# Optimization experiments

Measured on AMD Instinct MI355X. Metric: run time of the kernel, lower is better.

Reference implementation:

```python
import jax, jax.numpy as jnp
import numpy as np
from jax import lax

H = 512      # hidden_size (== embed dim)
K = 128      # attr_size
V = 32000    # output_size (vocab)
ANUM = 20    # aspect_num = len(aspect_ids)//100
N, B = 64, 32
T, S, A = 256, 32, 5


def setup_inputs() -> dict:
    key = jax.random.key(0)
    ks = jax.random.split(key, 32)
    f = lambda i, shape, s=0.02: (jax.random.normal(ks[i], shape, jnp.float32) * s)
    inp = {
        "input_seq": jax.random.randint(ks[0], (N, B), 0, V, jnp.int32),
        "last_hidden": jax.random.normal(ks[1], (1, B, H), jnp.float32),
        "encoder_out1": jax.random.normal(ks[2], (T, B, H), jnp.float32),
        "encoder_out2": jax.random.normal(ks[3], (S, B, H), jnp.float32),
        "encoder_out3": jax.random.normal(ks[4], (A, B, K), jnp.float32),
        "encoder_out4": jax.random.normal(ks[5], (A, B, ANUM), jnp.float32),
        "aspect_ids": jax.random.randint(ks[6], (100 * ANUM,), 0, V, jnp.int32),
        # learned parameters
        "emb": f(7, (V, H)),
        "gru_Wih": f(8, (3 * H, H)), "gru_Whh": f(9, (3 * H, H)),
        "gru_bih": f(10, (3 * H,)), "gru_bhh": f(11, (3 * H,)),
        "attn_W": f(12, (H, 2 * H)), "attn_b": f(13, (H,)), "attn_v": f(14, (H,)),
        "attr_W": f(15, (H, H + K)), "attr_b": f(16, (H,)), "attr_v": f(17, (H,)),
        "concat_W": f(18, (H, 3 * H + K)), "concat_b": f(19, (H,)),
        "out_W": f(20, (V, H)), "out_b": f(21, (V,)),
        "gate_W": f(22, (ANUM, 2 * H + ANUM)), "gate_b": f(23, (ANUM,)),
        "proj_W": f(24, (ANUM, 2 * ANUM)), "proj_b": f(25, (ANUM,)),
    }
    return inp


def _gru(x, h0, Wih, Whh, bih, bhh):
    # x: (N,B,H); h0: (B,H). PyTorch gate order: reset, update, new.
    def step(h, xt):
        gi = xt @ Wih.T + bih
        gh = h @ Whh.T + bhh
        ir, iz, inn = jnp.split(gi, 3, axis=-1)
        hr, hz, hn = jnp.split(gh, 3, axis=-1)
        r = jax.nn.sigmoid(ir + hr)
        z = jax.nn.sigmoid(iz + hz)
        n = jnp.tanh(inn + r * hn)
        h_new = (1.0 - z) * n + z * h
        return h_new, h_new
    hT, ys = lax.scan(step, h0, x)
    return ys, hT


def _attn(hidden, enc, W, b, v):
    # Faithful to Attn/AttributeAttn: energies[b,n,t] = tanh(v . (W @ cat(hidden[n,b], enc[t,b]) + b))
    # W @ cat = hidden @ Wh^T + enc @ We^T; dot with v distributes -> avoid (T,N,B,*) blowup.
    Hh = hidden.shape[-1]
    Wh, We = W[:, :Hh], W[:, Hh:]
    a = hidden @ (Wh.T @ v) + jnp.dot(b, v)   # (N,B)
    c = enc @ (We.T @ v)                       # (T,B)
    e = jnp.tanh(a.T[:, :, None] + c.T[:, None, :])  # (B,N,T)
    return jax.nn.softmax(e, axis=2)


def reference(input_seq, last_hidden, encoder_out1, encoder_out2, encoder_out3,
              encoder_out4, aspect_ids, emb, gru_Wih, gru_Whh, gru_bih, gru_bhh,
              attn_W, attn_b, attn_v, attr_W, attr_b, attr_v, concat_W, concat_b,
              out_W, out_b, gate_W, gate_b, proj_W, proj_b):
    seq_len = input_seq.shape[0]
    embedded = emb[input_seq]                                   # (N,B,H), dropout=eval noop
    rnn_output, hT = _gru(embedded, last_hidden[0], gru_Wih, gru_Whh, gru_bih, gru_bhh)
    hidden = hT[None]                                           # (1,B,H)

    aw1 = _attn(rnn_output, encoder_out1, attn_W, attn_b, attn_v)   # (B,N,T)
    ctx1 = jnp.einsum('bnt,tbh->nbh', aw1, encoder_out1)
    aw2 = _attn(rnn_output, encoder_out2, attn_W, attn_b, attn_v)   # (B,N,S)
    ctx2 = jnp.einsum('bns,sbh->nbh', aw2, encoder_out2)
    aw3 = _attn(rnn_output, encoder_out3, attr_W, attr_b, attr_v)   # (B,N,A)
    ctx3 = jnp.einsum('bna,abk->nbk', aw3, encoder_out3)

    concat_input = jnp.concatenate([rnn_output, ctx1, ctx2, ctx3], axis=2)
    concat_output = jnp.tanh(concat_input @ concat_W.T + concat_b)  # (N,B,H)
    output = concat_output @ out_W.T + out_b                        # (N,B,V)

    e4 = jnp.concatenate([encoder_out4[0], encoder_out4[1]], axis=-1)  # (B,2*ANUM)
    e4 = e4 @ proj_W.T + proj_b                                        # (B,ANUM)
    e4 = jnp.broadcast_to(e4[None], (seq_len,) + e4.shape)             # (N,B,ANUM)

    gate = jnp.tanh(jnp.concatenate([embedded, rnn_output, e4], axis=2) @ gate_W.T + gate_b)
    vals = jnp.tile(gate, (1, 1, 100))                                 # (N,B,100*ANUM)
    output = output.at[:, :, aspect_ids].add(vals)
    return output, hidden, aw1, aw2, aw3, gate
```

## Files before the change

kernel.cpp:

```cpp
#include <hip/hip_runtime.h>
#include <hip/hip_bf16.h>

#define HDIM 512
#define KA   128
#define VOC  32000
#define ANUMC 20
#define NSEQ 64
#define BATCH 32
#define TLEN 256
#define SLEN 32
#define ALEN 5
#define NB   2048
#define CIN  1664
#define G3H  1536
#define GB   64

typedef __bf16 bf16;
typedef bf16 v8bf __attribute__((ext_vector_type(8)));
typedef float v4f __attribute__((ext_vector_type(4)));

#define DEV __device__ __forceinline__

DEV float sigmoidf_(float x) { return 1.f / (1.f + expf(-x)); }

__global__ void k_zero(int* bar) {
  for (int i = threadIdx.x; i < GB * 32; i += 256) bar[i] = 0;
}

__global__ void k_init0(float* addtab, int* colnz) {
  int i = blockIdx.x * 256 + threadIdx.x;
  if (i < VOC * ANUMC) addtab[i] = 0.f;
  if (i < VOC) colnz[i] = 0;
}
__global__ void k_init1(const int* __restrict__ ids, float* addtab, int* colnz) {
  for (int k = threadIdx.x; k < 2000; k += 256) {
    int j = ids[k];
    atomicAdd(addtab + (size_t)j * ANUMC + (k % ANUMC), 1.0f);
    colnz[j] = 1;
  }
}

__global__ void k_vec(const float* __restrict__ attn_W, const float* __restrict__ attn_b,
                      const float* __restrict__ attn_v,
                      const float* __restrict__ attr_W, const float* __restrict__ attr_b,
                      const float* __restrict__ attr_v,
                      const float* __restrict__ enc4, const float* __restrict__ pW,
                      const float* __restrict__ pb, float* __restrict__ misc) {
  int tid = threadIdx.x;
  int blk = blockIdx.x;
  if (blk == 0) {
    for (int i = tid; i < 512; i += 256) {
      float s = 0.f;
      for (int j = 0; j < 512; ++j) s += attn_W[j * 1024 + i] * attn_v[j];
      misc[i] = s;
    }
  } else if (blk == 1) {
    for (int i = tid; i < 512; i += 256) {
      float s = 0.f;
      for (int j = 0; j < 512; ++j) s += attn_W[j * 1024 + 512 + i] * attn_v[j];
      misc[512 + i] = s;
    }
  } else if (blk == 2) {
    for (int i = tid; i < 512; i += 256) {
      float s = 0.f;
      for (int j = 0; j < 512; ++j) s += attr_W[j * 640 + i] * attr_v[j];
      misc[1024 + i] = s;
    }
  } else {
    for (int i = tid; i < 128; i += 256) {
      float s = 0.f;
      for (int j = 0; j < 512; ++j) s += attr_W[j * 640 + 512 + i] * attr_v[j];
      misc[1536 + i] = s;
    }
    if (tid == 128) {
      float s = 0.f;
      for (int j = 0; j < 512; ++j) s += attn_b[j] * attn_v[j];
      misc[1664] = s;
    }
    if (tid == 129) {
      float s = 0.f;
      for (int j = 0; j < 512; ++j) s += attr_b[j] * attr_v[j];
      misc[1665] = s;
    }
    for (int i = tid; i < BATCH * ANUMC; i += 256) {
      int b = i / ANUMC, j = i % ANUMC;
      float s = pb[j];
      for (int q = 0; q < ANUMC; ++q) s += pW[j * 40 + q] * enc4[b * ANUMC + q];
      for (int q = 0; q < ANUMC; ++q) s += pW[j * 40 + 20 + q] * enc4[BATCH * ANUMC + b * ANUMC + q];
      misc[1792 + i] = s;
    }
  }
}

__global__ void k_embcvt(const int* __restrict__ seq, const float* __restrict__ emb,
                         float* __restrict__ embedded, bf16* __restrict__ emb_bf,
                         const float* __restrict__ Wih, bf16* __restrict__ Wih_bf,
                         const float* __restrict__ cW, bf16* __restrict__ cW_bf,
                         const float* __restrict__ oW, bf16* __restrict__ oW_bf) {
  size_t i = (size_t)blockIdx.x * 256 + threadIdx.x;
  const size_t s0 = 1048576, s1 = s0 + 786432, s2 = s1 + 851968, s3 = s2 + 16384000;
  if (i < s0) {
    int row = (int)(i >> 9), col = (int)(i & 511);
    float v = emb[(size_t)seq[row] * 512 + col];
    embedded[i] = v;
    emb_bf[i] = (bf16)v;
  } else if (i < s1) {
    size_t j = i - s0;
    Wih_bf[j] = (bf16)Wih[j];
  } else if (i < s2) {
    size_t j = i - s1;
    cW_bf[j] = (bf16)cW[j];
  } else if (i < s3) {
    size_t j = i - s2;
    oW_bf[j] = (bf16)oW[j];
  }
}

__global__ void k_c(const float* __restrict__ enc1, const float* __restrict__ enc2,
                    const float* __restrict__ enc3, float* __restrict__ misc) {
  int i = blockIdx.x * 256 + threadIdx.x;
  const float* u1e = misc + 512;
  const float* u3e = misc + 1536;
  if (i < 8192) {
    const float* row = enc1 + (size_t)i * 512;
    float s = 0.f;
#pragma unroll 4
    for (int j = 0; j < 512; j += 4) {
      float4 a = *(const float4*)(row + j);
      float4 u = *(const float4*)(u1e + j);
      s += a.x * u.x + a.y * u.y + a.z * u.z + a.w * u.w;
    }
    misc[2560 + i] = s;
  } else if (i < 8192 + 1024) {
    int k = i - 8192;
    const float* row = enc2 + (size_t)k * 512;
    float s = 0.f;
#pragma unroll 4
    for (int j = 0; j < 512; j += 4) {
      float4 a = *(const float4*)(row + j);
      float4 u = *(const float4*)(u1e + j);
      s += a.x * u.x + a.y * u.y + a.z * u.z + a.w * u.w;
    }
    misc[10752 + k] = s;
  } else if (i < 8192 + 1024 + 160) {
    int k = i - 9216;
    const float* row = enc3 + (size_t)k * 128;
    float s = 0.f;
#pragma unroll 4
    for (int j = 0; j < 128; j += 4) {
      float4 a = *(const float4*)(row + j);
      float4 u = *(const float4*)(u3e + j);
      s += a.x * u.x + a.y * u.y + a.z * u.z + a.w * u.w;
    }
    misc[11776 + k] = s;
  }
}

template <int EPI>
__global__ __launch_bounds__(256, 2) void k_gemm_bt(const bf16* __restrict__ A,
                                                    const bf16* __restrict__ Bm,
                                                    const float* __restrict__ bias,
                                                    float* __restrict__ Cf, bf16* __restrict__ Cb,
                                                    int M, int Nn, int Kd,
                                                    const float* __restrict__ addtab,
                                                    const int* __restrict__ colnz,
                                                    const float* __restrict__ gate) {
  __shared__ __align__(16) unsigned short As[128 * 64];
  __shared__ __align__(16) unsigned short Bs[128 * 64];
  int tid = threadIdx.x;
  int nwg = gridDim.x;
  int cpx = nwg >> 3;
  int wgid = (blockIdx.x & 7) * cpx + (blockIdx.x >> 3);
  int MT = M >> 7;
  int m0 = (wgid % MT) << 7;
  int n0 = (wgid / MT) << 7;
  int lane = tid & 63;
  int wv = tid >> 6;
  int wm = wv & 1, wn = wv >> 1;
  int l15 = lane & 15, quad = lane >> 4;
  int l8r = lane >> 3;
  int lp = lane & 7;

  v4f acc[4][4];
#pragma unroll
  for (int i = 0; i < 4; ++i)
#pragma unroll
    for (int j = 0; j < 4; ++j) acc[i][j] = (v4f){0.f, 0.f, 0.f, 0.f};

  for (int kb = 0; kb < Kd; kb += 64) {
#pragma unroll
    for (int r = 0; r < 4; ++r) {
      int g = wv * 4 + r;
      int lr = g * 8 + l8r;
      int ca = (lp ^ (lr & 7)) * 8;
      __builtin_amdgcn_global_load_lds(
          (const __attribute__((address_space(1))) void*)(A + (size_t)(m0 + lr) * Kd + kb + ca),
          (__attribute__((address_space(3))) void*)((char*)As + g * 1024), 16, 0, 0);
      __builtin_amdgcn_global_load_lds(
          (const __attribute__((address_space(1))) void*)(Bm + (size_t)(n0 + lr) * Kd + kb + ca),
          (__attribute__((address_space(3))) void*)((char*)Bs + g * 1024), 16, 0, 0);
    }
    __syncthreads();
#pragma unroll
    for (int ks = 0; ks < 2; ++ks) {
      v8bf af[4], bfr[4];
      int c = ks * 4 + quad;
#pragma unroll
      for (int i = 0; i < 4; ++i) {
        int mr = wm * 64 + i * 16 + l15;
        af[i] = *(const v8bf*)((const char*)As + mr * 128 + ((c ^ (mr & 7)) << 4));
      }
#pragma unroll
      for (int j = 0; j < 4; ++j) {
        int nr = wn * 64 + j * 16 + l15;
        bfr[j] = *(const v8bf*)((const char*)Bs + nr * 128 + ((c ^ (nr & 7)) << 4));
      }
#pragma unroll
      for (int i = 0; i < 4; ++i)
#pragma unroll
        for (int j = 0; j < 4; ++j)
          acc[i][j] = __builtin_amdgcn_mfma_f32_16x16x32_bf16(af[i], bfr[j], acc[i][j], 0, 0, 0);
    }
    __syncthreads();
  }
#pragma unroll
  for (int i = 0; i < 4; ++i) {
    int gr0 = m0 + wm * 64 + i * 16 + quad * 4;
#pragma unroll
    for (int j = 0; j < 4; ++j) {
      int gc = n0 + wn * 64 + j * 16 + l15;
      float bs = bias[gc];
      if (EPI == 2) {
        int nz = colnz[gc];
        float ar[ANUMC];
        if (nz) {
#pragma unroll
          for (int a = 0; a < ANUMC; ++a) ar[a] = addtab[(size_t)gc * ANUMC + a];
        }
#pragma unroll
        for (int reg = 0; reg < 4; ++reg) {
          float v = acc[i][j][reg] + bs;
          if (nz) {
            const float* gr = gate + (size_t)(gr0 + reg) * ANUMC;
#pragma unroll
            for (int a = 0; a < ANUMC; ++a) v += ar[a] * gr[a];
          }
          Cf[(size_t)(gr0 + reg) * Nn + gc] = v;
        }
      } else {
#pragma unroll
        for (int reg = 0; reg < 4; ++reg) {
          float v = acc[i][j][reg] + bs;
          if (EPI == 1)
            Cb[(size_t)(gr0 + reg) * Nn + gc] = (bf16)tanhf(v);
          else
            Cf[(size_t)(gr0 + reg) * Nn + gc] = v;
        }
      }
    }
  }
}

__global__ __launch_bounds__(256) void k_gru(const float* __restrict__ gi,
                                             const float* __restrict__ Whh,
                                             const float* __restrict__ bhh,
                                             const float* __restrict__ lasth,
                                             float* __restrict__ rnn,
                                             bf16* __restrict__ concat_bf,
                                             unsigned long long* __restrict__ hx,
                                             int* __restrict__ bar) {
  struct SMEM {
    unsigned short hs[32 * 512];
    float gh[32 * 29];
    unsigned short hnew[256];
    int go;
  };
  __shared__ __align__(16) SMEM sm;
  int tid = threadIdx.x;
  int blk = blockIdx.x;
  int c0 = blk * 8;

  int lane = tid & 63;
  int w = tid >> 6;
  int l15 = lane & 15, quad = lane >> 4;
  int m0 = (w & 1) * 16;
  int n0 = (w >> 1) * 16;

  if (tid == 0) sm.go = 0;

  v8bf breg[16];
  {
    int nr = n0 + l15;
    if (nr > 23) nr = 23;
    const float* wrow = Whh + (size_t)((nr >> 3) * 512 + c0 + (nr & 7)) * 512;
#pragma unroll
    for (int it = 0; it < 16; ++it) {
      int k0 = it * 32 + quad * 8;
      float4 x = *(const float4*)(wrow + k0);
      float4 y = *(const float4*)(wrow + k0 + 4);
      v8bf vv;
      vv[0] = (bf16)x.x; vv[1] = (bf16)x.y; vv[2] = (bf16)x.z; vv[3] = (bf16)x.w;
      vv[4] = (bf16)y.x; vv[5] = (bf16)y.y; vv[6] = (bf16)y.z; vv[7] = (bf16)y.w;
      breg[it] = vv;
    }
  }

#pragma unroll
  for (int rnd = 0; rnd < 8; ++rnd) {
    int ch = rnd * 256 + tid;
    int bb = ch >> 6, cc = ch & 63;
    const float* hp = lasth + bb * 512 + cc * 8;
    float4 x = *(const float4*)hp;
    float4 y = *(const float4*)(hp + 4);
    v8bf vv;
    vv[0] = (bf16)x.x; vv[1] = (bf16)x.y; vv[2] = (bf16)x.z; vv[3] = (bf16)x.w;
    vv[4] = (bf16)y.x; vv[5] = (bf16)y.y; vv[6] = (bf16)y.z; vv[7] = (bf16)y.w;
    *(v8bf*)((char*)sm.hs + bb * 1024 + ((cc ^ (bb & 7)) << 4)) = vv;
  }

  int cb = tid >> 3, j = tid & 7, c = c0 + j;
  float hprev = lasth[cb * 512 + c];
  float b_r = bhh[c], b_z = bhh[512 + c], b_n = bhh[1024 + c];
  __syncthreads();

  for (int t = 0; t < 64; ++t) {
    const float* gii = gi + ((size_t)t * 32 + cb) * G3H;
    float g_r = gii[c];
    float g_z = gii[512 + c];
    float g_n = gii[1024 + c];

    {
      v4f acc0 = (v4f){0.f, 0.f, 0.f, 0.f};
      v4f acc1 = (v4f){0.f, 0.f, 0.f, 0.f};
      int mr = m0 + l15;
#pragma unroll
      for (int it = 0; it < 8; ++it) {
        {
          int ccx = it * 4 + quad;
          v8bf af = *(const v8bf*)((const char*)sm.hs + mr * 1024 + ((ccx ^ (mr & 7)) << 4));
          acc0 = __builtin_amdgcn_mfma_f32_16x16x32_bf16(af, breg[it], acc0, 0, 0, 0);
        }
        {
          int ccx = (it + 8) * 4 + quad;
          v8bf af = *(const v8bf*)((const char*)sm.hs + mr * 1024 + ((ccx ^ (mr & 7)) << 4));
          acc1 = __builtin_amdgcn_mfma_f32_16x16x32_bf16(af, breg[it + 8], acc1, 0, 0, 0);
        }
      }
      v4f acc = acc0 + acc1;
      if (n0 == 0 || l15 < 8) {
#pragma unroll
        for (int reg = 0; reg < 4; ++reg)
          sm.gh[(m0 + quad * 4 + reg) * 29 + n0 + l15] = acc[reg];
      }
    }
    __syncthreads();

    {
      float ar = sm.gh[cb * 29 + j] + b_r;
      float az = sm.gh[cb * 29 + 8 + j] + b_z;
      float an = sm.gh[cb * 29 + 16 + j] + b_n;
      float rg = sigmoidf_(g_r + ar);
      float zg = sigmoidf_(g_z + az);
      float ng = tanhf(g_n + rg * an);
      float hn = (1.f - zg) * ng + zg * hprev;
      hprev = hn;
      rnn[((size_t)t * 32 + cb) * 512 + c] = hn;
      bf16 hb = (bf16)hn;
      concat_bf[((size_t)t * 32 + cb) * CIN + c] = hb;
      sm.hnew[tid] = *(unsigned short*)&hb;
    }

    if (t < 63) {
      __syncthreads();
      int target = t + 1;
      int pnext = target & 1;
      if (w == 0) {
        unsigned long long pk = *(const unsigned long long*)(sm.hnew + lane * 4);
        int wd = (lane >> 1) * 128 + blk * 2 + (lane & 1);
        __hip_atomic_store(hx + (size_t)pnext * 4096 + wd, pk,
                           __ATOMIC_RELAXED, __HIP_MEMORY_SCOPE_AGENT);
        asm volatile("s_waitcnt vmcnt(0)" ::: "memory");
        if (lane == 0)
          __hip_atomic_store(&bar[blk * 32], target, __ATOMIC_RELAXED,
                             __HIP_MEMORY_SCOPE_AGENT);
        for (;;) {
          int v = __hip_atomic_load(&bar[lane * 32], __ATOMIC_RELAXED,
                                    __HIP_MEMORY_SCOPE_AGENT);
          if (__all(v >= target)) break;
          __builtin_amdgcn_s_sleep(1);
        }
        if (lane == 0) *(volatile int*)&sm.go = target;
      } else {
        while (*(volatile int*)&sm.go < target) __builtin_amdgcn_s_sleep(1);
      }

      {
        const unsigned long long* src = hx + (size_t)pnext * 4096 + w * 1024 + lane;
        unsigned long long vv[16];
#pragma unroll
        for (int i = 0; i < 16; ++i)
          vv[i] = __hip_atomic_load(src + i * 64, __ATOMIC_RELAXED,
                                    __HIP_MEMORY_SCOPE_AGENT);
#pragma unroll
        for (int i = 0; i < 16; ++i) {
          int W = w * 1024 + i * 64 + lane;
          int bb = W >> 7, wr = W & 127;
          int u = wr >> 1, half = wr & 1;
          *(unsigned long long*)((char*)sm.hs + bb * 1024 +
                                 (((u ^ (bb & 7)) << 4) | (half << 3))) = vv[i];
        }
      }
      __syncthreads();
    }
  }
}

__global__ __launch_bounds__(256) void k_attnrow(const float* __restrict__ rnn,
                                                 const float* __restrict__ misc,
                                                 float* __restrict__ aw1,
                                                 float* __restrict__ aw2,
                                                 float* __restrict__ aw3) {
  int wv = (blockIdx.x * 256 + threadIdx.x) >> 6;
  int lane = threadIdx.x & 63;
  if (wv >= 2048) return;
  int n = wv >> 5, b = wv & 31;
  const float* u1a = misc;
  const float* u3h = misc + 1024;
  const float* c1 = misc + 2560;
  const float* c2 = misc + 10752;
  const float* c3 = misc + 11776;
  const float* row = rnn + (size_t)(n * 32 + b) * 512;
  float s1 = 0.f, s3 = 0.f;
#pragma unroll
  for (int q = 0; q < 8; ++q) {
    int j = lane * 8 + q;
    float rv = row[j];
    s1 += rv * u1a[j];
    s3 += rv * u3h[j];
  }
  for (int o = 32; o > 0; o >>= 1) {
    s1 += __shfl_down(s1, o);
    s3 += __shfl_down(s3, o);
  }
  s1 = __shfl(s1, 0) + misc[1664];
  s3 = __shfl(s3, 0) + misc[1665];

  float e[4];
  float mx = -1e30f;
#pragma unroll
  for (int q = 0; q < 4; ++q) {
    int t = q * 64 + lane;
    e[q] = tanhf(s1 + c1[t * 32 + b]);
    mx = fmaxf(mx, e[q]);
  }
  for (int o = 32; o > 0; o >>= 1) mx = fmaxf(mx, __shfl_xor(mx, o));
  float sum = 0.f;
#pragma unroll
  for (int q = 0; q < 4; ++q) {
    e[q] = expf(e[q] - mx);
    sum += e[q];
  }
  for (int o = 32; o > 0; o >>= 1) sum += __shfl_xor(sum, o);
  float inv = 1.f / sum;
  size_t base1 = (size_t)(b * 64 + n) * 256;
#pragma unroll
  for (int q = 0; q < 4; ++q) aw1[base1 + q * 64 + lane] = e[q] * inv;

  float e2 = (lane < 32) ? tanhf(s1 + c2[lane * 32 + b]) : -1e30f;
  float m2 = e2;
  for (int o = 32; o > 0; o >>= 1) m2 = fmaxf(m2, __shfl_xor(m2, o));
  float x2 = (lane < 32) ? expf(e2 - m2) : 0.f;
  float sm2 = x2;
  for (int o = 32; o > 0; o >>= 1) sm2 += __shfl_xor(sm2, o);
  if (lane < 32) aw2[(size_t)(b * 64 + n) * 32 + lane] = x2 / sm2;

  float e3 = (lane < 5) ? tanhf(s3 + c3[lane * 32 + b]) : -1e30f;
  float m3 = e3;
  for (int o = 32; o > 0; o >>= 1) m3 = fmaxf(m3, __shfl_xor(m3, o));
  float x3 = (lane < 5) ? expf(e3 - m3) : 0.f;
  float sm3 = x3;
  for (int o = 32; o > 0; o >>= 1) sm3 += __shfl_xor(sm3, o);
  if (lane < 5) aw3[(size_t)(b * 64 + n) * 5 + lane] = x3 / sm3;
}

template <int TL, int COFF>
__global__ __launch_bounds__(256) void k_ctx(const float* __restrict__ aw,
                                             const float* __restrict__ enc,
                                             bf16* __restrict__ concat_bf) {
  __shared__ __align__(16) float awsT[TL * 36];
  int tid = threadIdx.x;
  int bx = blockIdx.x;
  int b = bx >> 2, q = (bx >> 1) & 1, nh = bx & 1;
  for (int i = tid; i < 32 * TL; i += 256) {
    int n = i / TL, te = i % TL;
    awsT[te * 36 + n] = aw[(size_t)b * 64 * TL + (size_t)(nh * 32 + n) * TL + te];
  }
  __syncthreads();
  int col = q * 256 + tid;
  float4 acc[8];
#pragma unroll
  for (int n4 = 0; n4 < 8; ++n4) acc[n4] = make_float4(0.f, 0.f, 0.f, 0.f);
  for (int te = 0; te < TL; ++te) {
    float v = enc[((size_t)te * 32 + b) * 512 + col];
#pragma unroll
    for (int n4 = 0; n4 < 8; ++n4) {
      float4 wv = *(const float4*)(awsT + te * 36 + n4 * 4);
      acc[n4].x += wv.x * v;
      acc[n4].y += wv.y * v;
      acc[n4].z += wv.z * v;
      acc[n4].w += wv.w * v;
    }
  }
#pragma unroll
  for (int n4 = 0; n4 < 8; ++n4) {
    int ng = nh * 32 + n4 * 4;
    concat_bf[((size_t)(ng + 0) * 32 + b) * CIN + COFF + col] = (bf16)acc[n4].x;
    concat_bf[((size_t)(ng + 1) * 32 + b) * CIN + COFF + col] = (bf16)acc[n4].y;
    concat_bf[((size_t)(ng + 2) * 32 + b) * CIN + COFF + col] = (bf16)acc[n4].z;
    concat_bf[((size_t)(ng + 3) * 32 + b) * CIN + COFF + col] = (bf16)acc[n4].w;
  }
}

__global__ void k_ctx3_misc(const float* __restrict__ aw3, const float* __restrict__ enc3,
                            const float* __restrict__ rnn, bf16* __restrict__ concat_bf,
                            float* __restrict__ hid) {
  int i = blockIdx.x * 256 + threadIdx.x;
  if (i < NB * 128) {
    int row = i >> 7, k = i & 127;
    int n = row >> 5, b = row & 31;
    float s = 0.f;
#pragma unroll
    for (int a = 0; a < 5; ++a)
      s += aw3[(size_t)(b * 64 + n) * 5 + a] * enc3[((size_t)a * 32 + b) * 128 + k];
    concat_bf[(size_t)row * CIN + 1536 + k] = (bf16)s;
  } else {
    int j = i - NB * 128;
    if (j < 16384) hid[j] = rnn[(size_t)63 * 16384 + j];
  }
}

__global__ __launch_bounds__(256) void k_gate(const float* __restrict__ embedded,
                                              const float* __restrict__ rnn,
                                              const float* __restrict__ misc,
                                              const float* __restrict__ gW,
                                              const float* __restrict__ gb,
                                              float* __restrict__ gate) {
  int i = blockIdx.x * 256 + threadIdx.x;
  if (i >= NB * ANUMC) return;
  int row = i / ANUMC, j = i % ANUMC;
  int b = row & 31;
  const float* w = gW + (size_t)j * 1044;
  const float* e = embedded + (size_t)row * 512;
  const float* r = rnn + (size_t)row * 512;
  float s = gb[j];
#pragma unroll 4
  for (int k = 0; k < 512; k += 4) {
    float4 a = *(const float4*)(e + k);
    float4 ww = *(const float4*)(w + k);
    s += a.x * ww.x + a.y * ww.y + a.z * ww.z + a.w * ww.w;
  }
#pragma unroll 4
  for (int k = 0; k < 512; k += 4) {
    float4 a = *(const float4*)(r + k);
    float4 ww = *(const float4*)(w + 512 + k);
    s += a.x * ww.x + a.y * ww.y + a.z * ww.z + a.w * ww.w;
  }
  const float* e4 = misc + 1792 + b * ANUMC;
#pragma unroll
  for (int q = 0; q < ANUMC; ++q) s += w[1024 + q] * e4[q];
  gate[i] = tanhf(s);
}

extern "C" void kernel_launch(void* const* d_in, const int* in_sizes, int n_in,
                              void* d_out, int out_size, void* d_ws, size_t ws_size,
                              hipStream_t stream) {
  const int* seq = (const int*)d_in[0];
  const float* lasth = (const float*)d_in[1];
  const float* enc1 = (const float*)d_in[2];
  const float* enc2 = (const float*)d_in[3];
  const float* enc3 = (const float*)d_in[4];
  const float* enc4 = (const float*)d_in[5];
  const int* aspect = (const int*)d_in[6];
  const float* emb = (const float*)d_in[7];
  const float* Wih = (const float*)d_in[8];
  const float* Whh = (const float*)d_in[9];
  const float* bih = (const float*)d_in[10];
  const float* bhh = (const float*)d_in[11];
  const float* attn_W = (const float*)d_in[12];
  const float* attn_b = (const float*)d_in[13];
  const float* attn_v = (const float*)d_in[14];
  const float* attr_W = (const float*)d_in[15];
  const float* attr_b = (const float*)d_in[16];
  const float* attr_v = (const float*)d_in[17];
  const float* cW = (const float*)d_in[18];
  const float* cbias = (const float*)d_in[19];
  const float* oW = (const float*)d_in[20];
  const float* ob = (const float*)d_in[21];
  const float* gW = (const float*)d_in[22];
  const float* gb = (const float*)d_in[23];
  const float* pW = (const float*)d_in[24];
  const float* pb = (const float*)d_in[25];

  char* ws = (char*)d_ws;
  float* misc = (float*)(ws + 0);
  float* embedded = (float*)(ws + 65536);
  float* gi = (float*)(ws + 4259840);
  float* rnn = (float*)(ws + 16842752);
  bf16* emb_bf = (bf16*)(ws + 21037056);
  bf16* Wih_bf = (bf16*)(ws + 23134208);
  bf16* cW_bf = (bf16*)(ws + 24707072);
  bf16* oW_bf = (bf16*)(ws + 26411008);
  bf16* concat_bf = (bf16*)(ws + 59179008);
  bf16* cout_bf = (bf16*)(ws + 65994752);
  unsigned long long* hx = (unsigned long long*)(ws + 68091904);
  int* bar = (int*)(misc + 12032);
  float* addtab = (float*)(ws + 4259840);
  int* colnz = (int*)(ws + 4259840 + 2560000);

  float* out = (float*)d_out;
  float* hid_out = out + 65536000;
  float* aw1 = out + 65552384;
  float* aw2 = out + 66076672;
  float* aw3 = out + 66142208;
  float* gate = out + 66152448;

  k_zero<<<1, 256, 0, stream>>>(bar);
  k_vec<<<4, 256, 0, stream>>>(attn_W, attn_b, attn_v, attr_W, attr_b, attr_v, enc4, pW, pb, misc);
  k_embcvt<<<74496, 256, 0, stream>>>(seq, emb, embedded, emb_bf, Wih, Wih_bf, cW, cW_bf, oW,
                                      oW_bf);
  k_c<<<37, 256, 0, stream>>>(enc1, enc2, enc3, misc);
  k_gemm_bt<0><<<192, 256, 0, stream>>>(emb_bf, Wih_bf, bih, gi, nullptr, NB, G3H, 512,
                                        nullptr, nullptr, nullptr);
  k_gru<<<GB, 256, 0, stream>>>(gi, Whh, bhh, lasth, rnn, concat_bf, hx, bar);
  k_init0<<<2625, 256, 0, stream>>>(addtab, colnz);
  k_init1<<<1, 256, 0, stream>>>(aspect, addtab, colnz);
  k_attnrow<<<512, 256, 0, stream>>>(rnn, misc, aw1, aw2, aw3);
  k_ctx<256, 512><<<128, 256, 0, stream>>>(aw1, enc1, concat_bf);
  k_ctx<32, 1024><<<128, 256, 0, stream>>>(aw2, enc2, concat_bf);
  k_ctx3_misc<<<1088, 256, 0, stream>>>(aw3, enc3, rnn, concat_bf, hid_out);
  k_gate<<<160, 256, 0, stream>>>(embedded, rnn, misc, gW, gb, gate);
  k_gemm_bt<1><<<64, 256, 0, stream>>>(concat_bf, cW_bf, cbias, nullptr, cout_bf, NB,
                                       512, CIN, nullptr, nullptr, nullptr);
  k_gemm_bt<2><<<4000, 256, 0, stream>>>(cout_bf, oW_bf, ob, out, nullptr, NB, VOC, 512,
                                         addtab, colnz, gate);
}
```

Measured before the change: 1.050 ms.

## Read GRU hidden state straight from global into MFMA fragments; vectorize bf16 conversion

The GRU recurrence no longer stages the exchanged hidden state through a swizzled LDS buffer behind a wave-0 barrier plus LDS flag handshake. Every wave now polls the per-block step counters itself and loads its bf16 A-fragments directly from the global double buffer. The initial hidden state is packed into that buffer by k_zero, which now runs extra blocks for it. Separately, the embedding gather and weight fp32-to-bf16 conversion kernel is vectorized to 4 elements per thread with packed 64-bit stores. The aim is to shorten the per-step synchronization critical path and cut instruction count in the conversion pass. The cost is more global polling traffic and redundant fragment loads per wave, and the spin loop has no sleep.

```diff
diff --git a/kernel.cpp b/kernel.cpp
--- a/kernel.cpp
+++ b/kernel.cpp
@@ -23,8 +23,24 @@
 
 DEV float sigmoidf_(float x) { return 1.f / (1.f + expf(-x)); }
 
-__global__ void k_zero(int* bar) {
-  for (int i = threadIdx.x; i < GB * 32; i += 256) bar[i] = 0;
+DEV unsigned long long pack4bf(float a, float b, float c, float d) {
+  bf16 b0 = (bf16)a, b1 = (bf16)b, b2 = (bf16)c, b3 = (bf16)d;
+  return (unsigned long long)*(unsigned short*)&b0 |
+         ((unsigned long long)*(unsigned short*)&b1 << 16) |
+         ((unsigned long long)*(unsigned short*)&b2 << 32) |
+         ((unsigned long long)*(unsigned short*)&b3 << 48);
+}
+
+__global__ void k_zero(int* bar, const float* __restrict__ lasth,
+                       unsigned long long* __restrict__ hx) {
+  if (blockIdx.x == 0) {
+    for (int i = threadIdx.x; i < GB * 32; i += 256) bar[i] = 0;
+  } else {
+    int w = (blockIdx.x - 1) * 256 + threadIdx.x;
+    int batch = w >> 7, c4 = w & 127;
+    float4 v = *(const float4*)(lasth + batch * 512 + c4 * 4);
+    hx[w] = pack4bf(v.x, v.y, v.z, v.w);
+  }
 }
 
 __global__ void k_init0(float* addtab, int* colnz) {
@@ -97,22 +113,25 @@
                          const float* __restrict__ Wih, bf16* __restrict__ Wih_bf,
                          const float* __restrict__ cW, bf16* __restrict__ cW_bf,
                          const float* __restrict__ oW, bf16* __restrict__ oW_bf) {
-  size_t i = (size_t)blockIdx.x * 256 + threadIdx.x;
+  size_t i = ((size_t)blockIdx.x * 256 + threadIdx.x) * 4;
   const size_t s0 = 1048576, s1 = s0 + 786432, s2 = s1 + 851968, s3 = s2 + 16384000;
   if (i < s0) {
     int row = (int)(i >> 9), col = (int)(i & 511);
-    float v = emb[(size_t)seq[row] * 512 + col];
-    embedded[i] = v;
-    emb_bf[i] = (bf16)v;
+    float4 v = *(const float4*)(emb + (size_t)seq[row] * 512 + col);
+    *(float4*)(embedded + i) = v;
+    *(unsigned long long*)(emb_bf + i) = pack4bf(v.x, v.y, v.z, v.w);
   } else if (i < s1) {
     size_t j = i - s0;
-    Wih_bf[j] = (bf16)Wih[j];
+    float4 v = *(const float4*)(Wih + j);
+    *(unsigned long long*)(Wih_bf + j) = pack4bf(v.x, v.y, v.z, v.w);
   } else if (i < s2) {
     size_t j = i - s1;
-    cW_bf[j] = (bf16)cW[j];
+    float4 v = *(const float4*)(cW + j);
+    *(unsigned long long*)(cW_bf + j) = pack4bf(v.x, v.y, v.z, v.w);
   } else if (i < s3) {
     size_t j = i - s2;
-    oW_bf[j] = (bf16)oW[j];
+    float4 v = *(const float4*)(oW + j);
+    *(unsigned long long*)(oW_bf + j) = pack4bf(v.x, v.y, v.z, v.w);
   }
 }
 
@@ -270,10 +289,8 @@
                                              unsigned long long* __restrict__ hx,
                                              int* __restrict__ bar) {
   struct SMEM {
-    unsigned short hs[32 * 512];
     float gh[32 * 29];
     unsigned short hnew[256];
-    int go;
   };
   __shared__ __align__(16) SMEM sm;
   int tid = threadIdx.x;
@@ -285,8 +302,6 @@
   int l15 = lane & 15, quad = lane >> 4;
   int m0 = (w & 1) * 16;
   int n0 = (w >> 1) * 16;
-
-  if (tid == 0) sm.go = 0;
 
   v8bf breg[16];
   {
@@ -305,23 +320,9 @@
     }
   }
 
-#pragma unroll
-  for (int rnd = 0; rnd < 8; ++rnd) {
-    int ch = rnd * 256 + tid;
-    int bb = ch >> 6, cc = ch & 63;
-    const float* hp = lasth + bb * 512 + cc * 8;
-    float4 x = *(const float4*)hp;
-    float4 y = *(const float4*)(hp + 4);
-    v8bf vv;
-    vv[0] = (bf16)x.x; vv[1] = (bf16)x.y; vv[2] = (bf16)x.z; vv[3] = (bf16)x.w;
-    vv[4] = (bf16)y.x; vv[5] = (bf16)y.y; vv[6] = (bf16)y.z; vv[7] = (bf16)y.w;
-    *(v8bf*)((char*)sm.hs + bb * 1024 + ((cc ^ (bb & 7)) << 4)) = vv;
-  }
-
   int cb = tid >> 3, j = tid & 7, c = c0 + j;
   float hprev = lasth[cb * 512 + c];
   float b_r = bhh[c], b_z = bhh[512 + c], b_n = bhh[1024 + c];
-  __syncthreads();
 
   for (int t = 0; t < 64; ++t) {
     const float* gii = gi + ((size_t)t * 32 + cb) * G3H;
@@ -330,21 +331,37 @@
     float g_n = gii[1024 + c];
 
     {
+      int v0 = __hip_atomic_load(&bar[lane * 32], __ATOMIC_RELAXED, __HIP_MEMORY_SCOPE_AGENT);
+      int v1 = __hip_atomic_load(&bar[lane * 32], __ATOMIC_RELAXED, __HIP_MEMORY_SCOPE_AGENT);
+      for (;;) {
+        if (__all(v0 >= t)) break;
+        v0 = __hip_atomic_load(&bar[lane * 32], __ATOMIC_RELAXED, __HIP_MEMORY_SCOPE_AGENT);
+        if (__all(v1 >= t)) break;
+        v1 = __hip_atomic_load(&bar[lane * 32], __ATOMIC_RELAXED, __HIP_MEMORY_SCOPE_AGENT);
+      }
+    }
+
+    const unsigned long long* hb =
+        hx + (size_t)(t & 1) * 4096 + (size_t)(m0 + l15) * 128 + quad * 2;
+    v8bf fr[16];
+#pragma unroll
+    for (int it = 0; it < 16; ++it) {
+      unsigned long long a0 =
+          __hip_atomic_load(hb + it * 8, __ATOMIC_RELAXED, __HIP_MEMORY_SCOPE_AGENT);
+      unsigned long long a1 =
+          __hip_atomic_load(hb + it * 8 + 1, __ATOMIC_RELAXED, __HIP_MEMORY_SCOPE_AGENT);
+      union { unsigned long long q[2]; v8bf v; } u;
+      u.q[0] = a0; u.q[1] = a1;
+      fr[it] = u.v;
+    }
+
+    {
       v4f acc0 = (v4f){0.f, 0.f, 0.f, 0.f};
       v4f acc1 = (v4f){0.f, 0.f, 0.f, 0.f};
-      int mr = m0 + l15;
 #pragma unroll
       for (int it = 0; it < 8; ++it) {
-        {
-          int ccx = it * 4 + quad;
-          v8bf af = *(const v8bf*)((const char*)sm.hs + mr * 1024 + ((ccx ^ (mr & 7)) << 4));
-          acc0 = __builtin_amdgcn_mfma_f32_16x16x32_bf16(af, breg[it], acc0, 0, 0, 0);
-        }
-        {
-          int ccx = (it + 8) * 4 + quad;
-          v8bf af = *(const v8bf*)((const char*)sm.hs + mr * 1024 + ((ccx ^ (mr & 7)) << 4));
-          acc1 = __builtin_amdgcn_mfma_f32_16x16x32_bf16(af, breg[it + 8], acc1, 0, 0, 0);
-        }
+        acc0 = __builtin_amdgcn_mfma_f32_16x16x32_bf16(fr[it], breg[it], acc0, 0, 0, 0);
+        acc1 = __builtin_amdgcn_mfma_f32_16x16x32_bf16(fr[it + 8], breg[it + 8], acc1, 0, 0, 0);
       }
       v4f acc = acc0 + acc1;
       if (n0 == 0 || l15 < 8) {
@@ -365,52 +382,20 @@
       float hn = (1.f - zg) * ng + zg * hprev;
       hprev = hn;
       rnn[((size_t)t * 32 + cb) * 512 + c] = hn;
-      bf16 hb = (bf16)hn;
-      concat_bf[((size_t)t * 32 + cb) * CIN + c] = hb;
-      sm.hnew[tid] = *(unsigned short*)&hb;
-    }
-
-    if (t < 63) {
-      __syncthreads();
-      int target = t + 1;
-      int pnext = target & 1;
-      if (w == 0) {
-        unsigned long long pk = *(const unsigned long long*)(sm.hnew + lane * 4);
-        int wd = (lane >> 1) * 128 + blk * 2 + (lane & 1);
-        __hip_atomic_store(hx + (size_t)pnext * 4096 + wd, pk,
-                           __ATOMIC_RELAXED, __HIP_MEMORY_SCOPE_AGENT);
-        asm volatile("s_waitcnt vmcnt(0)" ::: "memory");
-        if (lane == 0)
-          __hip_atomic_store(&bar[blk * 32], target, __ATOMIC_RELAXED,
-                             __HIP_MEMORY_SCOPE_AGENT);
-        for (;;) {
-          int v = __hip_atomic_load(&bar[lane * 32], __ATOMIC_RELAXED,
-                                    __HIP_MEMORY_SCOPE_AGENT);
-          if (__all(v >= target)) break;
-          __builtin_amdgcn_s_sleep(1);
-        }
-        if (lane == 0) *(volatile int*)&sm.go = target;
-      } else {
-        while (*(volatile int*)&sm.go < target) __builtin_amdgcn_s_sleep(1);
-      }
-
-      {
-        const unsigned long long* src = hx + (size_t)pnext * 4096 + w * 1024 + lane;
-        unsigned long long vv[16];
-#pragma unroll
-        for (int i = 0; i < 16; ++i)
-          vv[i] = __hip_atomic_load(src + i * 64, __ATOMIC_RELAXED,
-                                    __HIP_MEMORY_SCOPE_AGENT);
-#pragma unroll
-        for (int i = 0; i < 16; ++i) {
-          int W = w * 1024 + i * 64 + lane;
-          int bb = W >> 7, wr = W & 127;
-          int u = wr >> 1, half = wr & 1;
-          *(unsigned long long*)((char*)sm.hs + bb * 1024 +
-                                 (((u ^ (bb & 7)) << 4) | (half << 3))) = vv[i];
-        }
-      }
-      __syncthreads();
+      bf16 hb2 = (bf16)hn;
+      concat_bf[((size_t)t * 32 + cb) * CIN + c] = hb2;
+      sm.hnew[tid] = *(unsigned short*)&hb2;
+    }
+    __syncthreads();
+
+    if (t < 63 && w == 0) {
+      int batch = lane >> 1, half = lane & 1;
+      unsigned long long pk = *(const unsigned long long*)(sm.hnew + batch * 8 + half * 4);
+      __hip_atomic_store(hx + (size_t)((t + 1) & 1) * 4096 + batch * 128 + blk * 2 + half, pk,
+                         __ATOMIC_RELAXED, __HIP_MEMORY_SCOPE_AGENT);
+      asm volatile("s_waitcnt vmcnt(0)" ::: "memory");
+      if (lane == 0)
+        __hip_atomic_store(&bar[blk * 32], t + 1, __ATOMIC_RELAXED, __HIP_MEMORY_SCOPE_AGENT);
     }
   }
 }
@@ -624,9 +609,9 @@
   float* aw3 = out + 66142208;
   float* gate = out + 66152448;
 
-  k_zero<<<1, 256, 0, stream>>>(bar);
+  k_zero<<<17, 256, 0, stream>>>(bar, lasth, hx);
   k_vec<<<4, 256, 0, stream>>>(attn_W, attn_b, attn_v, attr_W, attr_b, attr_v, enc4, pW, pb, misc);
-  k_embcvt<<<74496, 256, 0, stream>>>(seq, emb, embedded, emb_bf, Wih, Wih_bf, cW, cW_bf, oW,
+  k_embcvt<<<18624, 256, 0, stream>>>(seq, emb, embedded, emb_bf, Wih, Wih_bf, cW, cW_bf, oW,
                                       oW_bf);
   k_c<<<37, 256, 0, stream>>>(enc1, enc2, enc3, misc);
   k_gemm_bt<0><<<192, 256, 0, stream>>>(emb_bf, Wih_bf, bih, gi, nullptr, NB, G3H, 512,
```

New measurement: 1.217 ms. +15.9%, slower.

## Restructure GRU grid barrier with double-buffered hidden state and dedicated poll waves

Applied to the files above, without the earlier changes.

The persistent GRU kernel now runs 512 threads per block. Four waves do the MFMA recurrence and four extra waves publish the new hidden slice and spin on a packed barrier array, with every polling wave waiting itself instead of relaying through a shared flag. Hidden state in shared memory is double-buffered so the next step's slice can be loaded while the current one is still being read. The hx layout and barrier stride are changed, and the sleep in the spin loop is dropped. The embedding/weight bf16 conversion kernel is also vectorised to four elements per thread. The aims are lower per-step grid-synchronisation latency and fewer conversion threads, at the cost of more threads and more barrier polling traffic.

```diff
diff --git a/kernel.cpp b/kernel.cpp
--- a/kernel.cpp
+++ b/kernel.cpp
@@ -23,8 +23,16 @@
 
 DEV float sigmoidf_(float x) { return 1.f / (1.f + expf(-x)); }
 
+DEV unsigned long long pack4bf(float a, float b, float c, float d) {
+  bf16 b0 = (bf16)a, b1 = (bf16)b, b2 = (bf16)c, b3 = (bf16)d;
+  return (unsigned long long)*(unsigned short*)&b0 |
+         ((unsigned long long)*(unsigned short*)&b1 << 16) |
+         ((unsigned long long)*(unsigned short*)&b2 << 32) |
+         ((unsigned long long)*(unsigned short*)&b3 << 48);
+}
+
 __global__ void k_zero(int* bar) {
-  for (int i = threadIdx.x; i < GB * 32; i += 256) bar[i] = 0;
+  if (threadIdx.x < GB) bar[threadIdx.x] = 0;
 }
 
 __global__ void k_init0(float* addtab, int* colnz) {
@@ -97,22 +105,25 @@
                          const float* __restrict__ Wih, bf16* __restrict__ Wih_bf,
                          const float* __restrict__ cW, bf16* __restrict__ cW_bf,
                          const float* __restrict__ oW, bf16* __restrict__ oW_bf) {
-  size_t i = (size_t)blockIdx.x * 256 + threadIdx.x;
+  size_t i = ((size_t)blockIdx.x * 256 + threadIdx.x) * 4;
   const size_t s0 = 1048576, s1 = s0 + 786432, s2 = s1 + 851968, s3 = s2 + 16384000;
   if (i < s0) {
     int row = (int)(i >> 9), col = (int)(i & 511);
-    float v = emb[(size_t)seq[row] * 512 + col];
-    embedded[i] = v;
-    emb_bf[i] = (bf16)v;
+    float4 v = *(const float4*)(emb + (size_t)seq[row] * 512 + col);
+    *(float4*)(embedded + i) = v;
+    *(unsigned long long*)(emb_bf + i) = pack4bf(v.x, v.y, v.z, v.w);
   } else if (i < s1) {
     size_t j = i - s0;
-    Wih_bf[j] = (bf16)Wih[j];
+    float4 v = *(const float4*)(Wih + j);
+    *(unsigned long long*)(Wih_bf + j) = pack4bf(v.x, v.y, v.z, v.w);
   } else if (i < s2) {
     size_t j = i - s1;
-    cW_bf[j] = (bf16)cW[j];
+    float4 v = *(const float4*)(cW + j);
+    *(unsigned long long*)(cW_bf + j) = pack4bf(v.x, v.y, v.z, v.w);
   } else if (i < s3) {
     size_t j = i - s2;
-    oW_bf[j] = (bf16)oW[j];
+    float4 v = *(const float4*)(oW + j);
+    *(unsigned long long*)(oW_bf + j) = pack4bf(v.x, v.y, v.z, v.w);
   }
 }
 
@@ -261,7 +272,7 @@
   }
 }
 
-__global__ __launch_bounds__(256) void k_gru(const float* __restrict__ gi,
+__global__ __launch_bounds__(512) void k_gru(const float* __restrict__ gi,
                                              const float* __restrict__ Whh,
                                              const float* __restrict__ bhh,
                                              const float* __restrict__ lasth,
@@ -270,10 +281,9 @@
                                              unsigned long long* __restrict__ hx,
                                              int* __restrict__ bar) {
   struct SMEM {
-    unsigned short hs[32 * 512];
+    unsigned short hs[2][32 * 512];
     float gh[32 * 29];
     unsigned short hnew[256];
-    int go;
   };
   __shared__ __align__(16) SMEM sm;
   int tid = threadIdx.x;
@@ -283,13 +293,10 @@
   int lane = tid & 63;
   int w = tid >> 6;
   int l15 = lane & 15, quad = lane >> 4;
-  int m0 = (w & 1) * 16;
-  int n0 = (w >> 1) * 16;
-
-  if (tid == 0) sm.go = 0;
 
   v8bf breg[16];
-  {
+  if (w < 4) {
+    int n0 = (w >> 1) * 16;
     int nr = n0 + l15;
     if (nr > 23) nr = 23;
     const float* wrow = Whh + (size_t)((nr >> 3) * 512 + c0 + (nr & 7)) * 512;
@@ -306,8 +313,8 @@
   }
 
 #pragma unroll
-  for (int rnd = 0; rnd < 8; ++rnd) {
-    int ch = rnd * 256 + tid;
+  for (int rnd = 0; rnd < 4; ++rnd) {
+    int ch = rnd * 512 + tid;
     int bb = ch >> 6, cc = ch & 63;
     const float* hp = lasth + bb * 512 + cc * 8;
     float4 x = *(const float4*)hp;
@@ -315,21 +322,32 @@
     v8bf vv;
     vv[0] = (bf16)x.x; vv[1] = (bf16)x.y; vv[2] = (bf16)x.z; vv[3] = (bf16)x.w;
     vv[4] = (bf16)y.x; vv[5] = (bf16)y.y; vv[6] = (bf16)y.z; vv[7] = (bf16)y.w;
-    *(v8bf*)((char*)sm.hs + bb * 1024 + ((cc ^ (bb & 7)) << 4)) = vv;
+    *(v8bf*)((char*)sm.hs[0] + bb * 1024 + ((cc ^ (bb & 7)) << 4)) = vv;
   }
 
   int cb = tid >> 3, j = tid & 7, c = c0 + j;
-  float hprev = lasth[cb * 512 + c];
-  float b_r = bhh[c], b_z = bhh[512 + c], b_n = bhh[1024 + c];
+  float hprev = 0.f, b_r = 0.f, b_z = 0.f, b_n = 0.f;
+  if (tid < 256) {
+    hprev = lasth[cb * 512 + c];
+    b_r = bhh[c];
+    b_z = bhh[512 + c];
+    b_n = bhh[1024 + c];
+  }
   __syncthreads();
 
   for (int t = 0; t < 64; ++t) {
-    const float* gii = gi + ((size_t)t * 32 + cb) * G3H;
-    float g_r = gii[c];
-    float g_z = gii[512 + c];
-    float g_n = gii[1024 + c];
-
-    {
+    int par = t & 1;
+    float g_r = 0.f, g_z = 0.f, g_n = 0.f;
+    if (tid < 256) {
+      const float* gii = gi + ((size_t)t * 32 + cb) * G3H;
+      g_r = gii[c];
+      g_z = gii[512 + c];
+      g_n = gii[1024 + c];
+    }
+
+    if (w < 4) {
+      int m0 = (w & 1) * 16;
+      int n0 = (w >> 1) * 16;
       v4f acc0 = (v4f){0.f, 0.f, 0.f, 0.f};
       v4f acc1 = (v4f){0.f, 0.f, 0.f, 0.f};
       int mr = m0 + l15;
@@ -337,12 +355,12 @@
       for (int it = 0; it < 8; ++it) {
         {
           int ccx = it * 4 + quad;
-          v8bf af = *(const v8bf*)((const char*)sm.hs + mr * 1024 + ((ccx ^ (mr & 7)) << 4));
+          v8bf af = *(const v8bf*)((const char*)sm.hs[par] + mr * 1024 + ((ccx ^ (mr & 7)) << 4));
           acc0 = __builtin_amdgcn_mfma_f32_16x16x32_bf16(af, breg[it], acc0, 0, 0, 0);
         }
         {
           int ccx = (it + 8) * 4 + quad;
-          v8bf af = *(const v8bf*)((const char*)sm.hs + mr * 1024 + ((ccx ^ (mr & 7)) << 4));
+          v8bf af = *(const v8bf*)((const char*)sm.hs[par] + mr * 1024 + ((ccx ^ (mr & 7)) << 4));
           acc1 = __builtin_amdgcn_mfma_f32_16x16x32_bf16(af, breg[it + 8], acc1, 0, 0, 0);
         }
       }
@@ -355,59 +373,55 @@
     }
     __syncthreads();
 
-    {
+    float hn = 0.f;
+    if (tid < 256) {
       float ar = sm.gh[cb * 29 + j] + b_r;
       float az = sm.gh[cb * 29 + 8 + j] + b_z;
       float an = sm.gh[cb * 29 + 16 + j] + b_n;
       float rg = sigmoidf_(g_r + ar);
       float zg = sigmoidf_(g_z + az);
       float ng = tanhf(g_n + rg * an);
-      float hn = (1.f - zg) * ng + zg * hprev;
+      hn = (1.f - zg) * ng + zg * hprev;
       hprev = hn;
+      bf16 hb = (bf16)hn;
+      sm.hnew[tid] = *(unsigned short*)&hb;
+    }
+    __syncthreads();
+
+    if (tid < 256) {
       rnn[((size_t)t * 32 + cb) * 512 + c] = hn;
-      bf16 hb = (bf16)hn;
-      concat_bf[((size_t)t * 32 + cb) * CIN + c] = hb;
-      sm.hnew[tid] = *(unsigned short*)&hb;
+      concat_bf[((size_t)t * 32 + cb) * CIN + c] = (bf16)hn;
     }
 
     if (t < 63) {
-      __syncthreads();
       int target = t + 1;
-      int pnext = target & 1;
-      if (w == 0) {
+      int p2 = target & 1;
+      if (w == 4) {
         unsigned long long pk = *(const unsigned long long*)(sm.hnew + lane * 4);
-        int wd = (lane >> 1) * 128 + blk * 2 + (lane & 1);
-        __hip_atomic_store(hx + (size_t)pnext * 4096 + wd, pk,
+        __hip_atomic_store(hx + (size_t)p2 * 4096 + blk * 64 + lane, pk,
                            __ATOMIC_RELAXED, __HIP_MEMORY_SCOPE_AGENT);
         asm volatile("s_waitcnt vmcnt(0)" ::: "memory");
         if (lane == 0)
-          __hip_atomic_store(&bar[blk * 32], target, __ATOMIC_RELAXED,
-                             __HIP_MEMORY_SCOPE_AGENT);
+          __hip_atomic_store(&bar[blk], target, __ATOMIC_RELAXED, __HIP_MEMORY_SCOPE_AGENT);
+      }
+      if (w >= 4) {
         for (;;) {
-          int v = __hip_atomic_load(&bar[lane * 32], __ATOMIC_RELAXED,
-                                    __HIP_MEMORY_SCOPE_AGENT);
+          int v = __hip_atomic_load(&bar[lane & 63], __ATOMIC_RELAXED, __HIP_MEMORY_SCOPE_AGENT);
           if (__all(v >= target)) break;
-          __builtin_amdgcn_s_sleep(1);
         }
-        if (lane == 0) *(volatile int*)&sm.go = target;
-      } else {
-        while (*(volatile int*)&sm.go < target) __builtin_amdgcn_s_sleep(1);
-      }
-
-      {
-        const unsigned long long* src = hx + (size_t)pnext * 4096 + w * 1024 + lane;
+        int wl = w - 4;
+        const unsigned long long* src = hx + (size_t)p2 * 4096 + wl * 1024 + lane;
         unsigned long long vv[16];
 #pragma unroll
         for (int i = 0; i < 16; ++i)
-          vv[i] = __hip_atomic_load(src + i * 64, __ATOMIC_RELAXED,
-                                    __HIP_MEMORY_SCOPE_AGENT);
+          vv[i] = __hip_atomic_load(src + i * 64, __ATOMIC_RELAXED, __HIP_MEMORY_SCOPE_AGENT);
 #pragma unroll
         for (int i = 0; i < 16; ++i) {
-          int W = w * 1024 + i * 64 + lane;
-          int bb = W >> 7, wr = W & 127;
-          int u = wr >> 1, half = wr & 1;
-          *(unsigned long long*)((char*)sm.hs + bb * 1024 +
-                                 (((u ^ (bb & 7)) << 4) | (half << 3))) = vv[i];
+          int idx = wl * 1024 + i * 64 + lane;
+          int p = idx >> 6, q = idx & 63;
+          int bb = q >> 1, half = q & 1;
+          *(unsigned long long*)((char*)sm.hs[p2] + bb * 1024 +
+                                 (((p ^ (bb & 7)) << 4) | (half << 3))) = vv[i];
         }
       }
       __syncthreads();
@@ -624,14 +638,14 @@
   float* aw3 = out + 66142208;
   float* gate = out + 66152448;
 
-  k_zero<<<1, 256, 0, stream>>>(bar);
+  k_zero<<<1, 64, 0, stream>>>(bar);
   k_vec<<<4, 256, 0, stream>>>(attn_W, attn_b, attn_v, attr_W, attr_b, attr_v, enc4, pW, pb, misc);
-  k_embcvt<<<74496, 256, 0, stream>>>(seq, emb, embedded, emb_bf, Wih, Wih_bf, cW, cW_bf, oW,
+  k_embcvt<<<18624, 256, 0, stream>>>(seq, emb, embedded, emb_bf, Wih, Wih_bf, cW, cW_bf, oW,
                                       oW_bf);
   k_c<<<37, 256, 0, stream>>>(enc1, enc2, enc3, misc);
   k_gemm_bt<0><<<192, 256, 0, stream>>>(emb_bf, Wih_bf, bih, gi, nullptr, NB, G3H, 512,
                                         nullptr, nullptr, nullptr);
-  k_gru<<<GB, 256, 0, stream>>>(gi, Whh, bhh, lasth, rnn, concat_bf, hx, bar);
+  k_gru<<<GB, 512, 0, stream>>>(gi, Whh, bhh, lasth, rnn, concat_bf, hx, bar);
   k_init0<<<2625, 256, 0, stream>>>(addtab, colnz);
   k_init1<<<1, 256, 0, stream>>>(aspect, addtab, colnz);
   k_attnrow<<<512, 256, 0, stream>>>(rnn, misc, aw1, aw2, aw3);
```

Result: slower. 1.083 ms (+3.1%).

## Vectorize weight conversion and compact GRU cross-block exchange and barrier layout

Applied to the files above, without the earlier changes.

The embedding gather and fp32-to-bf16 weight conversion kernel now handles four elements per thread with float4 loads and packed 64-bit bf16 stores, using a quarter of the blocks. In the persistent GRU kernel, the per-step hidden-state exchange buffer now uses a contiguous block-major layout with a simpler swizzled LDS scatter. The barrier flags are packed densely instead of being spaced 32 ints apart, and the global rnn/concat stores now sit after the barrier sync. Packing the flags puts all blocks' counters on shared cache lines, which could add contention while the poll loop needs fewer lines.

```diff
diff --git a/kernel.cpp b/kernel.cpp
--- a/kernel.cpp
+++ b/kernel.cpp
@@ -23,8 +23,16 @@
 
 DEV float sigmoidf_(float x) { return 1.f / (1.f + expf(-x)); }
 
+DEV unsigned long long pack4bf(float a, float b, float c, float d) {
+  bf16 b0 = (bf16)a, b1 = (bf16)b, b2 = (bf16)c, b3 = (bf16)d;
+  return (unsigned long long)*(unsigned short*)&b0 |
+         ((unsigned long long)*(unsigned short*)&b1 << 16) |
+         ((unsigned long long)*(unsigned short*)&b2 << 32) |
+         ((unsigned long long)*(unsigned short*)&b3 << 48);
+}
+
 __global__ void k_zero(int* bar) {
-  for (int i = threadIdx.x; i < GB * 32; i += 256) bar[i] = 0;
+  if (threadIdx.x < GB) bar[threadIdx.x] = 0;
 }
 
 __global__ void k_init0(float* addtab, int* colnz) {
@@ -97,22 +105,25 @@
                          const float* __restrict__ Wih, bf16* __restrict__ Wih_bf,
                          const float* __restrict__ cW, bf16* __restrict__ cW_bf,
                          const float* __restrict__ oW, bf16* __restrict__ oW_bf) {
-  size_t i = (size_t)blockIdx.x * 256 + threadIdx.x;
+  size_t i = ((size_t)blockIdx.x * 256 + threadIdx.x) * 4;
   const size_t s0 = 1048576, s1 = s0 + 786432, s2 = s1 + 851968, s3 = s2 + 16384000;
   if (i < s0) {
     int row = (int)(i >> 9), col = (int)(i & 511);
-    float v = emb[(size_t)seq[row] * 512 + col];
-    embedded[i] = v;
-    emb_bf[i] = (bf16)v;
+    float4 v = *(const float4*)(emb + (size_t)seq[row] * 512 + col);
+    *(float4*)(embedded + i) = v;
+    *(unsigned long long*)(emb_bf + i) = pack4bf(v.x, v.y, v.z, v.w);
   } else if (i < s1) {
     size_t j = i - s0;
-    Wih_bf[j] = (bf16)Wih[j];
+    float4 v = *(const float4*)(Wih + j);
+    *(unsigned long long*)(Wih_bf + j) = pack4bf(v.x, v.y, v.z, v.w);
   } else if (i < s2) {
     size_t j = i - s1;
-    cW_bf[j] = (bf16)cW[j];
+    float4 v = *(const float4*)(cW + j);
+    *(unsigned long long*)(cW_bf + j) = pack4bf(v.x, v.y, v.z, v.w);
   } else if (i < s3) {
     size_t j = i - s2;
-    oW_bf[j] = (bf16)oW[j];
+    float4 v = *(const float4*)(oW + j);
+    *(unsigned long long*)(oW_bf + j) = pack4bf(v.x, v.y, v.z, v.w);
   }
 }
 
@@ -355,6 +366,7 @@
     }
     __syncthreads();
 
+    float hn;
     {
       float ar = sm.gh[cb * 29 + j] + b_r;
       float az = sm.gh[cb * 29 + 8 + j] + b_z;
@@ -362,30 +374,28 @@
       float rg = sigmoidf_(g_r + ar);
       float zg = sigmoidf_(g_z + az);
       float ng = tanhf(g_n + rg * an);
-      float hn = (1.f - zg) * ng + zg * hprev;
+      hn = (1.f - zg) * ng + zg * hprev;
       hprev = hn;
-      rnn[((size_t)t * 32 + cb) * 512 + c] = hn;
       bf16 hb = (bf16)hn;
-      concat_bf[((size_t)t * 32 + cb) * CIN + c] = hb;
       sm.hnew[tid] = *(unsigned short*)&hb;
     }
+    __syncthreads();
+
+    rnn[((size_t)t * 32 + cb) * 512 + c] = hn;
+    concat_bf[((size_t)t * 32 + cb) * CIN + c] = (bf16)hn;
 
     if (t < 63) {
-      __syncthreads();
       int target = t + 1;
-      int pnext = target & 1;
+      int p2 = target & 1;
       if (w == 0) {
         unsigned long long pk = *(const unsigned long long*)(sm.hnew + lane * 4);
-        int wd = (lane >> 1) * 128 + blk * 2 + (lane & 1);
-        __hip_atomic_store(hx + (size_t)pnext * 4096 + wd, pk,
+        __hip_atomic_store(hx + (size_t)p2 * 4096 + blk * 64 + lane, pk,
                            __ATOMIC_RELAXED, __HIP_MEMORY_SCOPE_AGENT);
         asm volatile("s_waitcnt vmcnt(0)" ::: "memory");
         if (lane == 0)
-          __hip_atomic_store(&bar[blk * 32], target, __ATOMIC_RELAXED,
-                             __HIP_MEMORY_SCOPE_AGENT);
+          __hip_atomic_store(&bar[blk], target, __ATOMIC_RELAXED, __HIP_MEMORY_SCOPE_AGENT);
         for (;;) {
-          int v = __hip_atomic_load(&bar[lane * 32], __ATOMIC_RELAXED,
-                                    __HIP_MEMORY_SCOPE_AGENT);
+          int v = __hip_atomic_load(&bar[lane], __ATOMIC_RELAXED, __HIP_MEMORY_SCOPE_AGENT);
           if (__all(v >= target)) break;
           __builtin_amdgcn_s_sleep(1);
         }
@@ -395,19 +405,18 @@
       }
 
       {
-        const unsigned long long* src = hx + (size_t)pnext * 4096 + w * 1024 + lane;
+        const unsigned long long* src = hx + (size_t)p2 * 4096 + w * 1024 + lane;
         unsigned long long vv[16];
 #pragma unroll
         for (int i = 0; i < 16; ++i)
-          vv[i] = __hip_atomic_load(src + i * 64, __ATOMIC_RELAXED,
-                                    __HIP_MEMORY_SCOPE_AGENT);
+          vv[i] = __hip_atomic_load(src + i * 64, __ATOMIC_RELAXED, __HIP_MEMORY_SCOPE_AGENT);
 #pragma unroll
         for (int i = 0; i < 16; ++i) {
-          int W = w * 1024 + i * 64 + lane;
-          int bb = W >> 7, wr = W & 127;
-          int u = wr >> 1, half = wr & 1;
+          int p = w * 16 + i;
+          int bb = lane >> 1;
+          int half = lane & 1;
           *(unsigned long long*)((char*)sm.hs + bb * 1024 +
-                                 (((u ^ (bb & 7)) << 4) | (half << 3))) = vv[i];
+                                 (((p ^ (bb & 7)) << 4) | (half << 3))) = vv[i];
         }
       }
       __syncthreads();
@@ -624,9 +633,9 @@
   float* aw3 = out + 66142208;
   float* gate = out + 66152448;
 
-  k_zero<<<1, 256, 0, stream>>>(bar);
+  k_zero<<<1, 64, 0, stream>>>(bar);
   k_vec<<<4, 256, 0, stream>>>(attn_W, attn_b, attn_v, attr_W, attr_b, attr_v, enc4, pW, pb, misc);
-  k_embcvt<<<74496, 256, 0, stream>>>(seq, emb, embedded, emb_bf, Wih, Wih_bf, cW, cW_bf, oW,
+  k_embcvt<<<18624, 256, 0, stream>>>(seq, emb, embedded, emb_bf, Wih, Wih_bf, cW, cW_bf, oW,
                                       oW_bf);
   k_c<<<37, 256, 0, stream>>>(enc1, enc2, enc3, misc);
   k_gemm_bt<0><<<192, 256, 0, stream>>>(emb_bf, Wih_bf, bih, gi, nullptr, NB, G3H, 512,
```

Result: slower. 1.101 ms (+4.8%).
